# Kernel tuning notes

Measured on AMD Instinct MI355X. Metric: run time of the kernel, lower is better.

## Reference

```python
import jax, jax.numpy as jnp
import numpy as np

# ---- configuration (matches init_kwargs) ----
IH, IW, IC, OC = 32, 32, 8, 16
KH = KW = 3
STRIDE = (1, 1)
PAD = (1, 1)
DIL = (1, 1)
P = 5                       # num_gp_pts per GP neuron
I_DIM = IC * KH * KW        # 72 = kernel_input_size
OH = (IH + 2 * PAD[0] - DIL[0] * (KH - 1) - 1) // STRIDE[0] + 1
OW = (IW + 2 * PAD[1] - DIL[1] * (KW - 1) - 1) // STRIDE[1] + 1
JITTER = 1e-4


def setup_inputs() -> dict:
    key = jax.random.key(0)
    k1, k2, k3, k4, k5 = jax.random.split(key, 5)
    N = 8
    x_mean = jax.random.normal(k1, (N, IH, IW, IC), jnp.float32)
    # variances must be positive
    x_var = 0.1 + 0.9 * jax.random.uniform(k2, (N, IH, IW, IC), jnp.float32)
    # inducing inputs: spread on [-1,1] with small perturbation (well-conditioned K)
    base = jnp.linspace(-1.0, 1.0, P, dtype=jnp.float32)
    z = base[None, None, :] + 0.05 * jax.random.normal(k3, (OC, I_DIM, P), jnp.float32)
    h = jax.random.normal(k4, (OC, I_DIM, P), jnp.float32)      # inducing outputs
    raw_l = jax.random.uniform(k5, (OC, I_DIM), jnp.float32)    # pre-softplus lengthscale
    return {"x_mean": x_mean, "x_var": x_var, "z": z, "h": h, "raw_l": raw_l}


def im2col(img):
    """[N,IH,IW,C] NHWC -> [N*L, C*KH*KW], torch.nn.Unfold ordering (channel slowest)."""
    x = jnp.transpose(img, (0, 3, 1, 2))  # NCHW, matches the torch transposes
    patches = jax.lax.conv_general_dilated_patches(
        x, (KH, KW), STRIDE, [(PAD[0], PAD[0]), (PAD[1], PAD[1])], rhs_dilation=DIL
    )  # [N, C*KH*KW, OH, OW], feature dim channel-major like torch unfold
    Nb = patches.shape[0]
    return patches.reshape(Nb, I_DIM, OH * OW).transpose(0, 2, 1).reshape(Nb * OH * OW, I_DIM)


def gp_layer(mu, s2, z, h, raw_l):
    """GP-neuron (KAN-style) moment propagation.
    mu, s2: [R, I]; z, h: [O, I, P]; raw_l: [O, I].
    Per neuron (o,i): SE kernel k(a,b)=exp(-(a-b)^2/(2 l^2)), unit signal variance.
    Under x_i ~ N(mu_i, s2_i):
      q_p   = sqrt(l^2/(l^2+s2)) * exp(-(mu-z_p)^2 / (2 (l^2+s2)))   (expected kernel)
      mean  = q . K^{-1} h
      var   = 1 - q . K^{-1} q
    Layer output (KAN sum over inputs): y_o = sum_i f_oi(x_i).
    """
    l2 = jax.nn.softplus(raw_l) ** 2                                  # [O,I]
    dz = z[:, :, :, None] - z[:, :, None, :]                          # [O,I,P,P]
    K = jnp.exp(-0.5 * dz**2 / l2[:, :, None, None]) + JITTER * jnp.eye(P, dtype=mu.dtype)
    Kinv = jnp.linalg.inv(K)                                          # [O,I,P,P] (tiny)
    alpha = jnp.einsum('oipq,oiq->oip', Kinv, h)                      # [O,I,P]

    d = l2[None, :, :, None] + s2[:, None, :, None]                   # [R,O,I,1]
    diff = mu[:, None, :, None] - z[None]                             # [R,O,I,P]
    q = jnp.sqrt(l2[None, :, :, None] / d) * jnp.exp(-0.5 * diff**2 / d)  # [R,O,I,P]

    out_mean = jnp.einsum('roip,oip->ro', q, alpha)                   # [R,O]
    qK = jnp.einsum('roip,oipq->roiq', q, Kinv)                       # [R,O,I,P]
    qKq = jnp.einsum('roiq,roiq->ro', qK, q)                          # [R,O]
    # sum_i (k(x,x) - q K^{-1} q) with k(x,x)=1 -> I - sum_i qKq_i
    out_var = jnp.maximum(jnp.asarray(mu.shape[1], mu.dtype) - qKq, 1e-6)
    return out_mean, out_var


def reference(x_mean, x_var, z, h, raw_l):
    N = x_mean.shape[0]
    mu = im2col(x_mean)                  # [N*L, I]
    s2 = im2col(x_var)                   # [N*L, I]
    m, v = gp_layer(mu, s2, z, h, raw_l)
    # col2im: [N*L, OC] -> [N, OH, OW, OC]
    return m.reshape(N, OH, OW, OC), v.reshape(N, OH, OW, OC)
```

## Files before the change

### kernel.cpp

```cpp
#include <hip/hip_runtime.h>
#include <math.h>

#define OC_N   16
#define I_DIM  72
#define PN     5
#define NEU    (OC_N * I_DIM)
#define NF     32
#define RTOT   8192
#define OUT_HALF (RTOT * OC_N)
#define LOG2E  1.4426950408889634f
#define RLOG2E 0.6931471805599453f

#if __has_builtin(__builtin_amdgcn_rcpf)
#define RCPF(x) __builtin_amdgcn_rcpf(x)
#else
#define RCPF(x) (1.0f / (x))
#endif
#if __has_builtin(__builtin_amdgcn_exp2f)
#define EXP2F(x) __builtin_amdgcn_exp2f(x)
#else
#define EXP2F(x) exp2f(x)
#endif
#if __has_builtin(__builtin_amdgcn_logf)
#define LOG2F(x) __builtin_amdgcn_logf(x)
#else
#define LOG2F(x) log2f(x)
#endif


__global__ __launch_bounds__(256) void gp_prep_kernel(
    const float* __restrict__ zin, const float* __restrict__ hin,
    const float* __restrict__ rlin, float* __restrict__ nr) {
  int idx = blockIdx.x * blockDim.x + threadIdx.x;
  if (idx >= NEU) return;
  float x  = rlin[idx];
  float t  = EXP2F(-fabsf(x) * LOG2E);
  float sp = fmaxf(x, 0.0f) + LOG2F(1.0f + t) * RLOG2E;
  float l2 = sp * sp;
  float cexp = -0.5f * LOG2E * RCPF(l2);

  float zz[PN], hh[PN];
#pragma unroll
  for (int p = 0; p < PN; ++p) {
    zz[p] = zin[idx * PN + p];
    hh[p] = hin[idx * PN + p];
  }
  float A[PN][PN], B[PN][PN];
#pragma unroll
  for (int p = 0; p < PN; ++p) {
#pragma unroll
    for (int q = 0; q < PN; ++q) {
      float dz = zz[p] - zz[q];
      A[p][q] = EXP2F(cexp * dz * dz);
      B[p][q] = (p == q) ? 1.0f : 0.0f;
    }
  }
#pragma unroll
  for (int p = 0; p < PN; ++p) A[p][p] += 1e-4f;

#pragma unroll
  for (int c = 0; c < PN; ++c) {
    float pivinv = RCPF(A[c][c]);
#pragma unroll
    for (int j = 0; j < PN; ++j) { A[c][j] *= pivinv; B[c][j] *= pivinv; }
#pragma unroll
    for (int r = 0; r < PN; ++r) {
      if (r == c) continue;
      float f = A[r][c];
#pragma unroll
      for (int j = 0; j < PN; ++j) { A[r][j] -= f * A[c][j]; B[r][j] -= f * B[c][j]; }
    }
  }
  float alpha[PN];
#pragma unroll
  for (int p = 0; p < PN; ++p) {
    float s = 0.0f;
#pragma unroll
    for (int q = 0; q < PN; ++q) s += B[p][q] * hh[q];
    alpha[p] = s;
  }
  float* o = nr + idx * NF;
  o[0] = l2;
  o[1] = 0.0f;
#pragma unroll
  for (int p = 0; p < PN; ++p) {
    o[2 + p]  = zz[p];
    o[7 + p]  = alpha[p];
    o[12 + p] = B[p][p];
  }
  int j = 17;
#pragma unroll
  for (int p = 0; p < PN; ++p)
#pragma unroll
    for (int q = p + 1; q < PN; ++q) o[j++] = 2.0f * B[p][q];
  o[27] = o[28] = o[29] = o[30] = o[31] = 0.0f;
}

__global__ __launch_bounds__(576) void gp_fused_kernel(
    const float* __restrict__ xm, const float* __restrict__ xv,
    const float* __restrict__ nr, float* __restrict__ out) {
  const int tx  = threadIdx.x;
  const int rlo = tx >> 3;
  const int c   = tx & 7;
  const int k   = __builtin_amdgcn_readfirstlane(threadIdx.y);
  const int kh  = k / 3;
  const int kw  = k - kh * 3;
  const int o   = blockIdx.y;
  const int rbase = blockIdx.x * 64;

  const float* rec = nr + (o * I_DIM + (c * 9 + k)) * NF;
  float P[27];
#pragma unroll
  for (int j = 0; j < 27; ++j) P[j] = rec[j];

  const float l2    = P[0];
  __shared__ float2 red[9][64];

#pragma unroll
  for (int it = 0; it < 8; ++it) {
    const int r8  = rbase + it * 8;
    const int n   = r8 >> 10;
    const int pix = r8 & 1023;
    const int oh  = pix >> 5;
    const int ow0 = pix & 31;
    const int ih  = oh + kh - 1;
    const int iw  = ow0 + rlo + kw - 1;
    const bool valid = ((unsigned)ih < 32u) & ((unsigned)iw < 32u);
    const int ihc = ih < 0 ? 0 : (ih > 31 ? 31 : ih);
    const int iwc = iw < 0 ? 0 : (iw > 31 ? 31 : iw);
    const int addr = ((n * 32 + ihc) * 32 + iwc) * 8 + c;
    float m  = xm[addr];
    float s2 = xv[addr];
    m  = valid ? m  : 0.0f;
    s2 = valid ? s2 : 0.0f;

    const float d     = l2 + s2;
    const float inv_d = RCPF(d);
    const float coef2 = l2 * inv_d;
    const float coef  = sqrtf(coef2);
    const float el    = -0.72134752044f * inv_d;
    const float d0 = m - P[2];
    const float d1 = m - P[3];
    const float d2 = m - P[4];
    const float d3 = m - P[5];
    const float d4 = m - P[6];
    const float u0 = EXP2F(el * d0 * d0);
    const float u1 = EXP2F(el * d1 * d1);
    const float u2 = EXP2F(el * d2 * d2);
    const float u3 = EXP2F(el * d3 * d3);
    const float u4 = EXP2F(el * d4 * d4);
    const float dotA =
        fmaf(u0, P[7], fmaf(u1, P[8], fmaf(u2, P[9], fmaf(u3, P[10], u4 * P[11]))));
    const float t0 = fmaf(P[12], u0, fmaf(P[17], u1, fmaf(P[18], u2, fmaf(P[19], u3, P[20] * u4))));
    const float t1 = fmaf(P[13], u1, fmaf(P[21], u2, fmaf(P[22], u3, P[23] * u4)));
    const float t2 = fmaf(P[14], u2, fmaf(P[24], u3, P[25] * u4));
    const float t3 = fmaf(P[15], u3, P[26] * u4);
    const float t4 = P[16] * u4;
    const float quad =
        fmaf(u0, t0, fmaf(u1, t1, fmaf(u2, t2, fmaf(u3, t3, u4 * t4))));
    float mean = coef * dotA;
    float qkq  = coef2 * quad;

    mean += __shfl_xor(mean, 1); qkq += __shfl_xor(qkq, 1);
    mean += __shfl_xor(mean, 2); qkq += __shfl_xor(qkq, 2);
    mean += __shfl_xor(mean, 4); qkq += __shfl_xor(qkq, 4);
    if (c == 0) red[k][it * 8 + rlo] = make_float2(mean, qkq);
  }

  __syncthreads();
  if (threadIdx.y == 0) {
    float msum = 0.0f, qsum = 0.0f;
#pragma unroll
    for (int s = 0; s < 9; ++s) {
      const float2 v = red[s][tx];
      msum += v.x;
      qsum += v.y;
    }
    const int i = (rbase + tx) * OC_N + o;
    out[i] = msum;
    out[OUT_HALF + i] = fmaxf(72.0f - qsum, 1e-6f);
  }
}

extern "C" void kernel_launch(void* const* d_in, const int* in_sizes, int n_in,
                              void* d_out, int out_size, void* d_ws, size_t ws_size,
                              hipStream_t stream) {
  const float* xm = (const float*)d_in[0];
  const float* xv = (const float*)d_in[1];
  const float* z  = (const float*)d_in[2];
  const float* h  = (const float*)d_in[3];
  const float* rl = (const float*)d_in[4];
  float* out = (float*)d_out;
  float* nr  = (float*)d_ws;

  gp_prep_kernel<<<dim3((NEU + 255) / 256), dim3(256), 0, stream>>>(z, h, rl, nr);

  dim3 grid(RTOT / 64, OC_N);
  dim3 block(64, 9);
  gp_fused_kernel<<<grid, block, 0, stream>>>(xm, xv, nr, out);
}
```

Before: 99.54 us.

## Split kernel-offset reduction into separate pass via global partial buffer

The fused kernel, which reduced the nine kernel-offset partials through shared memory and a block barrier, is split in two. A main kernel puts each offset on its own grid z-slice and writes per-offset mean/qKq partials to workspace, and a small final kernel sums the nine partials and writes the outputs. The goal is to remove the block-wide sync and the 576-thread blocks in favour of smaller blocks with more occupancy. It also vectorises the parameter load as float4 and replaces sqrt with multiply-by-rsq. The cost is an extra launch plus a global round-trip of roughly 9x16x8192 float2 partials.

```diff
diff --git a/kernel.cpp b/kernel.cpp
--- a/kernel.cpp
+++ b/kernel.cpp
@@ -25,6 +25,11 @@
 #define LOG2F(x) __builtin_amdgcn_logf(x)
 #else
 #define LOG2F(x) log2f(x)
+#endif
+#if __has_builtin(__builtin_amdgcn_rsqf)
+#define RSQF(x) __builtin_amdgcn_rsqf(x)
+#else
+#define RSQF(x) rsqrtf(x)
 #endif
 
 
@@ -96,29 +101,31 @@
   o[27] = o[28] = o[29] = o[30] = o[31] = 0.0f;
 }
 
-__global__ __launch_bounds__(576) void gp_fused_kernel(
+__global__ __launch_bounds__(256, 2) void gp_main_kernel(
     const float* __restrict__ xm, const float* __restrict__ xv,
-    const float* __restrict__ nr, float* __restrict__ out) {
-  const int tx  = threadIdx.x;
-  const int rlo = tx >> 3;
-  const int c   = tx & 7;
-  const int k   = __builtin_amdgcn_readfirstlane(threadIdx.y);
-  const int kh  = k / 3;
-  const int kw  = k - kh * 3;
-  const int o   = blockIdx.y;
-  const int rbase = blockIdx.x * 64;
-
-  const float* rec = nr + (o * I_DIM + (c * 9 + k)) * NF;
-  float P[27];
-#pragma unroll
-  for (int j = 0; j < 27; ++j) P[j] = rec[j];
-
-  const float l2    = P[0];
-  __shared__ float2 red[9][64];
+    const float* __restrict__ nr, float2* __restrict__ pmq) {
+  const int tx   = threadIdx.x;
+  const int lane = tx & 63;
+  const int wy   = tx >> 6;
+  const int rlo  = lane >> 3;
+  const int c    = lane & 7;
+  const int k  = blockIdx.z;
+  const int kh = k / 3;
+  const int kw = k - kh * 3;
+  const int o  = blockIdx.y;
+  const int rblk = blockIdx.x * 256;
+
+  float P[28];
+  {
+    const float4* rec4 = (const float4*)(nr + (o * I_DIM + (c * 9 + k)) * NF);
+#pragma unroll
+    for (int j = 0; j < 7; ++j) *(float4*)&P[4 * j] = rec4[j];
+  }
+  const float l2 = P[0];
 
 #pragma unroll
   for (int it = 0; it < 8; ++it) {
-    const int r8  = rbase + it * 8;
+    const int r8  = rblk + it * 32 + wy * 8;
     const int n   = r8 >> 10;
     const int pix = r8 & 1023;
     const int oh  = pix >> 5;
@@ -129,15 +136,15 @@
     const int ihc = ih < 0 ? 0 : (ih > 31 ? 31 : ih);
     const int iwc = iw < 0 ? 0 : (iw > 31 ? 31 : iw);
     const int addr = ((n * 32 + ihc) * 32 + iwc) * 8 + c;
-    float m  = xm[addr];
-    float s2 = xv[addr];
-    m  = valid ? m  : 0.0f;
-    s2 = valid ? s2 : 0.0f;
-
-    const float d     = l2 + s2;
+    float m = xm[addr];
+    float s = xv[addr];
+    m = valid ? m : 0.0f;
+    s = valid ? s : 0.0f;
+
+    const float d     = l2 + s;
     const float inv_d = RCPF(d);
     const float coef2 = l2 * inv_d;
-    const float coef  = sqrtf(coef2);
+    const float coef  = coef2 * RSQF(coef2);
     const float el    = -0.72134752044f * inv_d;
     const float d0 = m - P[2];
     const float d1 = m - P[3];
@@ -164,22 +171,27 @@
     mean += __shfl_xor(mean, 1); qkq += __shfl_xor(qkq, 1);
     mean += __shfl_xor(mean, 2); qkq += __shfl_xor(qkq, 2);
     mean += __shfl_xor(mean, 4); qkq += __shfl_xor(qkq, 4);
-    if (c == 0) red[k][it * 8 + rlo] = make_float2(mean, qkq);
-  }
-
-  __syncthreads();
-  if (threadIdx.y == 0) {
-    float msum = 0.0f, qsum = 0.0f;
-#pragma unroll
-    for (int s = 0; s < 9; ++s) {
-      const float2 v = red[s][tx];
-      msum += v.x;
-      qsum += v.y;
-    }
-    const int i = (rbase + tx) * OC_N + o;
-    out[i] = msum;
-    out[OUT_HALF + i] = fmaxf(72.0f - qsum, 1e-6f);
-  }
+
+    if (c == 0)
+      pmq[(size_t)(k * OC_N + o) * RTOT + (r8 + rlo)] = make_float2(mean, qkq);
+  }
+}
+
+__global__ __launch_bounds__(256) void gp_final_kernel(
+    const float2* __restrict__ pmq, float* __restrict__ out) {
+  const int j = blockIdx.x * 256 + threadIdx.x;
+  const int o = j >> 13;
+  const int r = j & 8191;
+  float m = 0.0f, q = 0.0f;
+#pragma unroll
+  for (int s = 0; s < 9; ++s) {
+    const float2 v = pmq[(size_t)(s * OC_N + o) * RTOT + r];
+    m += v.x;
+    q += v.y;
+  }
+  const int i = r * OC_N + o;
+  out[i] = m;
+  out[OUT_HALF + i] = fmaxf(72.0f - q, 1e-6f);
 }
 
 extern "C" void kernel_launch(void* const* d_in, const int* in_sizes, int n_in,
@@ -191,11 +203,14 @@
   const float* h  = (const float*)d_in[3];
   const float* rl = (const float*)d_in[4];
   float* out = (float*)d_out;
-  float* nr  = (float*)d_ws;
+
+  float* nr   = (float*)d_ws;
+  float2* pmq = (float2*)((char*)d_ws + NEU * NF * 4);
 
   gp_prep_kernel<<<dim3((NEU + 255) / 256), dim3(256), 0, stream>>>(z, h, rl, nr);
 
-  dim3 grid(RTOT / 64, OC_N);
-  dim3 block(64, 9);
-  gp_fused_kernel<<<grid, block, 0, stream>>>(xm, xv, nr, out);
-}
+  dim3 grid(RTOT / 256, OC_N, 9);
+  gp_main_kernel<<<grid, dim3(256), 0, stream>>>(xm, xv, nr, pmq);
+
+  gp_final_kernel<<<dim3(OUT_HALF / 256), dim3(256), 0, stream>>>(pmq, out);
+}
```

After: 97.63 us. Within noise of the previous version (-1.9%).

## Stage input halo tile in LDS and use rsqrt for coefficient

Applied to the files above, without the earlier changes.

The fused kernel now loads the 4x34x8 halo tile of mean and variance into shared memory once per block, instead of each of the nine kernel-offset wavefront groups issuing its own clamped global loads. The sqrt/reciprocal pair is replaced by a single reciprocal square root, which works because the prep kernel now stores the softplus lengthscale itself. The per-neuron record is read with float4 loads, and launch bounds request two blocks per CU. The costs are an extra barrier and LDS traffic, plus slightly different rounding from rsq.

```diff
diff --git a/kernel.cpp b/kernel.cpp
--- a/kernel.cpp
+++ b/kernel.cpp
@@ -25,6 +25,11 @@
 #define LOG2F(x) __builtin_amdgcn_logf(x)
 #else
 #define LOG2F(x) log2f(x)
+#endif
+#if __has_builtin(__builtin_amdgcn_rsqf)
+#define RSQF(x) __builtin_amdgcn_rsqf(x)
+#else
+#define RSQF(x) rsqrtf(x)
 #endif
 
 
@@ -59,16 +64,16 @@
   for (int p = 0; p < PN; ++p) A[p][p] += 1e-4f;
 
 #pragma unroll
-  for (int c = 0; c < PN; ++c) {
-    float pivinv = RCPF(A[c][c]);
-#pragma unroll
-    for (int j = 0; j < PN; ++j) { A[c][j] *= pivinv; B[c][j] *= pivinv; }
+  for (int cc = 0; cc < PN; ++cc) {
+    float pivinv = RCPF(A[cc][cc]);
+#pragma unroll
+    for (int j = 0; j < PN; ++j) { A[cc][j] *= pivinv; B[cc][j] *= pivinv; }
 #pragma unroll
     for (int r = 0; r < PN; ++r) {
-      if (r == c) continue;
-      float f = A[r][c];
-#pragma unroll
-      for (int j = 0; j < PN; ++j) { A[r][j] -= f * A[c][j]; B[r][j] -= f * B[c][j]; }
+      if (r == cc) continue;
+      float f = A[r][cc];
+#pragma unroll
+      for (int j = 0; j < PN; ++j) { A[r][j] -= f * A[cc][j]; B[r][j] -= f * B[cc][j]; }
     }
   }
   float alpha[PN];
@@ -81,7 +86,7 @@
   }
   float* o = nr + idx * NF;
   o[0] = l2;
-  o[1] = 0.0f;
+  o[1] = sp;
 #pragma unroll
   for (int p = 0; p < PN; ++p) {
     o[2 + p]  = zz[p];
@@ -96,49 +101,68 @@
   o[27] = o[28] = o[29] = o[30] = o[31] = 0.0f;
 }
 
-__global__ __launch_bounds__(576) void gp_fused_kernel(
+__global__ __launch_bounds__(576, 2) void gp_fused_kernel(
     const float* __restrict__ xm, const float* __restrict__ xv,
     const float* __restrict__ nr, float* __restrict__ out) {
-  const int tx  = threadIdx.x;
-  const int rlo = tx >> 3;
-  const int c   = tx & 7;
-  const int k   = __builtin_amdgcn_readfirstlane(threadIdx.y);
-  const int kh  = k / 3;
-  const int kw  = k - kh * 3;
-  const int o   = blockIdx.y;
+  __shared__ float stage[2][4][34][8];
+  __shared__ float2 red[9][64];
+
+  const int tx   = threadIdx.x;
+  const int rlo  = tx >> 3;
+  const int c    = tx & 7;
+  const int k    = __builtin_amdgcn_readfirstlane(threadIdx.y);
+  const int kh   = k / 3;
+  const int kw   = k - 3 * kh;
+  const int o    = blockIdx.y;
   const int rbase = blockIdx.x * 64;
-
-  const float* rec = nr + (o * I_DIM + (c * 9 + k)) * NF;
-  float P[27];
-#pragma unroll
-  for (int j = 0; j < 27; ++j) P[j] = rec[j];
-
-  const float l2    = P[0];
-  __shared__ float2 red[9][64];
-
+  const int n    = rbase >> 10;
+  const int oh0  = (rbase & 1023) >> 5;
+
+  {
+    const int tid = threadIdx.y * 64 + tx;
+    float* flat = (float*)stage;
+    for (int idx = tid; idx < 2176; idx += 576) {
+      const int arr = idx / 1088;
+      const int rem = idx - arr * 1088;
+      const int j   = rem / 272;
+      const int f   = rem - j * 272;
+      const int pos = f >> 3;
+      const int cc  = f & 7;
+      const int iw  = pos - 1;
+      const int ih  = oh0 - 1 + j;
+      const bool valid = ((unsigned)ih < 32u) & ((unsigned)iw < 32u);
+      const int ihc = ih < 0 ? 0 : (ih > 31 ? 31 : ih);
+      const int iwc = iw < 0 ? 0 : (iw > 31 ? 31 : iw);
+      const float* g = arr ? xv : xm;
+      float v = g[((n * 32 + ihc) * 32 + iwc) * 8 + cc];
+      flat[idx] = valid ? v : 0.0f;
+    }
+  }
+
+  float P[28];
+  {
+    const float4* rec4 = (const float4*)(nr + (o * I_DIM + (c * 9 + k)) * NF);
+#pragma unroll
+    for (int j = 0; j < 7; ++j) ((float4*)P)[j] = rec4[j];
+  }
+  const float l2 = P[0];
+  const float l1 = P[1];
+
+  __syncthreads();
+
+  const int ih_l = kh;
 #pragma unroll
   for (int it = 0; it < 8; ++it) {
-    const int r8  = rbase + it * 8;
-    const int n   = r8 >> 10;
-    const int pix = r8 & 1023;
-    const int oh  = pix >> 5;
-    const int ow0 = pix & 31;
-    const int ih  = oh + kh - 1;
-    const int iw  = ow0 + rlo + kw - 1;
-    const bool valid = ((unsigned)ih < 32u) & ((unsigned)iw < 32u);
-    const int ihc = ih < 0 ? 0 : (ih > 31 ? 31 : ih);
-    const int iwc = iw < 0 ? 0 : (iw > 31 ? 31 : iw);
-    const int addr = ((n * 32 + ihc) * 32 + iwc) * 8 + c;
-    float m  = xm[addr];
-    float s2 = xv[addr];
-    m  = valid ? m  : 0.0f;
-    s2 = valid ? s2 : 0.0f;
-
-    const float d     = l2 + s2;
-    const float inv_d = RCPF(d);
-    const float coef2 = l2 * inv_d;
-    const float coef  = sqrtf(coef2);
-    const float el    = -0.72134752044f * inv_d;
+    const int oh_l = it >> 2;
+    const int ow0  = (it & 3) << 3;
+    const float m = stage[0][oh_l + ih_l][ow0 + kw + rlo][c];
+    const float s = stage[1][oh_l + ih_l][ow0 + kw + rlo][c];
+
+    const float d     = l2 + s;
+    const float irs   = RSQF(d);
+    const float coef  = l1 * irs;
+    const float coef2 = coef * coef;
+    const float el    = -0.72134752044f * (irs * irs);
     const float d0 = m - P[2];
     const float d1 = m - P[3];
     const float d2 = m - P[4];
```

New measurement: 95.83 us. 1.04x faster.
